# Kernel optimization log

Hardware: AMD Instinct MI355X
Metric: run time of the kernel (lower is better)

## Reference

```python
import jax, jax.numpy as jnp
import numpy as np
import math

B, T, D, H = 4, 2048, 1024, 16
HD = D // H  # head dim = 64

def setup_inputs() -> dict:
    key = jax.random.key(0)
    ks = jax.random.split(key, 4)
    scale = 1.0 / math.sqrt(D)
    return {
        "x": jax.random.normal(ks[0], (B, T, D), dtype=jnp.float32),
        "Wq": jax.random.normal(ks[1], (D, D), dtype=jnp.float32) * scale,
        "bq": jnp.zeros((D,), dtype=jnp.float32),
        "Wk": jax.random.normal(ks[2], (D, D), dtype=jnp.float32) * scale,
        "bk": jnp.zeros((D,), dtype=jnp.float32),
        "Wv": jax.random.normal(ks[3], (D, D), dtype=jnp.float32) * scale,
        "bv": jnp.zeros((D,), dtype=jnp.float32),
    }

def reference(x, Wq, bq, Wk, bk, Wv, bv):
    b, t, d = x.shape
    # QKV projections (nn.Dense): x @ W + b
    q = x @ Wq + bq
    k = x @ Wk + bk
    v = x @ Wv + bv
    # b n (h d) -> b h n d
    def split_heads(y):
        return y.reshape(b, t, H, HD).transpose(0, 2, 1, 3)
    q, k, v = split_heads(q), split_heads(k), split_heads(v)
    # scaled dot-product attention; scale by sqrt(features // heads)
    scores = jnp.einsum("bhqd,bhkd->bhqk", q, k) / math.sqrt(HD)
    attn = jax.nn.softmax(scores, axis=-1)
    # dropout rate 0.0 / eval mode => identity
    out = jnp.einsum("bhqk,bhkd->bhqd", attn, v)
    # b h n d -> b n (h d)
    return out.transpose(0, 2, 1, 3).reshape(b, t, d)
```

## Files before the change

kernel.cpp:

```cpp
#include <hip/hip_runtime.h>
#include <math.h>

typedef unsigned short u16;
typedef short short8 __attribute__((ext_vector_type(8)));
typedef u16 u16x4 __attribute__((ext_vector_type(4)));
typedef float f32x4 __attribute__((ext_vector_type(4)));
typedef __bf16 bf16x8 __attribute__((ext_vector_type(8)));

#define B_ 4
#define T_ 2048
#define D_ 1024
#define H_ 16
#define HD_ 64
#define BT_ 8192

__device__ __forceinline__ u16 f2bf(float f) {
  unsigned u = __builtin_bit_cast(unsigned, f);
  u = u + 0x7fffu + ((u >> 16) & 1u);
  return (u16)(u >> 16);
}
__device__ __forceinline__ f32x4 mfma16(short8 a, short8 b, f32x4 c) {
  return __builtin_amdgcn_mfma_f32_16x16x32_bf16(
      __builtin_bit_cast(bf16x8, a), __builtin_bit_cast(bf16x8, b), c, 0, 0, 0);
}
__device__ __forceinline__ void async16(u16* lds, const u16* g) {
  __builtin_amdgcn_global_load_lds(
      (const __attribute__((address_space(1))) unsigned int*)g,
      (__attribute__((address_space(3))) unsigned int*)lds, 16, 0, 0);
}

__global__ __launch_bounds__(256) void prep(
    const float* __restrict__ x, const float* __restrict__ Wq,
    const float* __restrict__ Wk, const float* __restrict__ Wv,
    u16* __restrict__ xbf, u16* __restrict__ wtq, u16* __restrict__ wtk,
    u16* __restrict__ wtv) {
  __shared__ float sh[32][33];
  if (blockIdx.y < 256) {
    int bid = blockIdx.y * 32 + blockIdx.x;
    int i = (bid * 256 + threadIdx.x) * 4;
    float4 v = *(const float4*)&x[i];
    u16x4 o = {f2bf(v.x), f2bf(v.y), f2bf(v.z), f2bf(v.w)};
    *(u16x4*)&xbf[i] = o;
    return;
  }
  const int yy = blockIdx.y - 256;
  const int wsel = yy >> 5;
  const float* in = (wsel == 0) ? Wq : (wsel == 1) ? Wk : Wv;
  u16* out = (wsel == 0) ? wtq : (wsel == 1) ? wtk : wtv;
  const int bx = blockIdx.x * 32, by = (yy & 31) * 32;
  const int col = threadIdx.x & 31, r8 = threadIdx.x >> 5;
#pragma unroll
  for (int i = 0; i < 4; i++) {
    int row = r8 + i * 8;
    sh[row][col] = in[(size_t)(by + row) * 1024 + bx + col];
  }
  __syncthreads();
#pragma unroll
  for (int i = 0; i < 4; i++) {
    int row = r8 + i * 8;
    out[(size_t)(bx + row) * 1024 + by + col] = f2bf(sh[col][row]);
  }
}

__global__ __launch_bounds__(256, 2) void gemm_qkv3(
    const u16* __restrict__ xbf, const u16* __restrict__ wtq,
    const u16* __restrict__ wtk, const u16* __restrict__ wtv,
    const float* __restrict__ bq, const float* __restrict__ bk,
    const float* __restrict__ bv, u16* __restrict__ qh, u16* __restrict__ kh,
    u16* __restrict__ vth, float qscale) {
  __shared__ __align__(16) u16 Rs[2][128 * 64];
  __shared__ __align__(16) u16 Cs[2][128 * 64];
  const int proj = blockIdx.y >> 3;
  const int fy = blockIdx.y & 7;
  const u16* Rm;
  const u16* Cm;
  const float* bias;
  u16* out;
  float scale;
  int r0, c0, vmode;
  if (proj == 0) {
    Rm = wtq; Cm = xbf; bias = bq; out = qh; scale = qscale; vmode = 0;
    r0 = fy * 128; c0 = blockIdx.x * 128;
  } else if (proj == 1) {
    Rm = wtk; Cm = xbf; bias = bk; out = kh; scale = 1.0f; vmode = 0;
    r0 = fy * 128; c0 = blockIdx.x * 128;
  } else {
    Rm = xbf; Cm = wtv; bias = bv; out = vth; scale = 1.0f; vmode = 1;
    r0 = blockIdx.x * 128; c0 = fy * 128;
  }
  const int tid = threadIdx.x;
  const int lane = tid & 63;
  const int w = tid >> 6;
  const int wr = w >> 1, wc = w & 1;
  const int c = lane & 15, q4 = lane >> 4;
  const int cx7 = c & 7;

  f32x4 acc[4][4];
#pragma unroll
  for (int i = 0; i < 4; i++)
#pragma unroll
    for (int j = 0; j < 4; j++) {
      f32x4 z = {0.f, 0.f, 0.f, 0.f};
      acc[i][j] = z;
    }

  const int sr = tid >> 3, pc = tid & 7;

#pragma unroll
  for (int i = 0; i < 4; i++) {
    int row = i * 32 + sr;
    int sc = (pc ^ (row & 7)) * 8;
    async16(&Rs[0][(i * 256 + tid) * 8], &Rm[(size_t)(r0 + row) * 1024 + sc]);
    async16(&Cs[0][(i * 256 + tid) * 8], &Cm[(size_t)(c0 + row) * 1024 + sc]);
  }

  for (int ks = 0; ks < 16; ks++) {
    const int cur = ks & 1;
    __syncthreads();
    if (ks + 1 < 16) {
      const int kk = (ks + 1) * 64;
#pragma unroll
      for (int i = 0; i < 4; i++) {
        int row = i * 32 + sr;
        int sc = (pc ^ (row & 7)) * 8;
        async16(&Rs[cur ^ 1][(i * 256 + tid) * 8],
                &Rm[(size_t)(r0 + row) * 1024 + kk + sc]);
        async16(&Cs[cur ^ 1][(i * 256 + tid) * 8],
                &Cm[(size_t)(c0 + row) * 1024 + kk + sc]);
      }
    }
#pragma unroll
    for (int h = 0; h < 2; h++) {
      short8 rF[4], cF[4];
      const int ko = ((h * 4 + q4) ^ cx7) * 8;
#pragma unroll
      for (int i = 0; i < 4; i++)
        rF[i] = *(const short8*)&Rs[cur][(wr * 64 + i * 16 + c) * 64 + ko];
#pragma unroll
      for (int j = 0; j < 4; j++)
        cF[j] = *(const short8*)&Cs[cur][(wc * 64 + j * 16 + c) * 64 + ko];
#pragma unroll
      for (int i = 0; i < 4; i++)
#pragma unroll
        for (int j = 0; j < 4; j++) acc[i][j] = mfma16(rF[i], cF[j], acc[i][j]);
    }
  }

  if (vmode == 0) {
#pragma unroll
    for (int i = 0; i < 4; i++) {
      int ng = r0 + wr * 64 + i * 16 + q4 * 4;
      int h = ng >> 6, hd = ng & 63;
#pragma unroll
      for (int j = 0; j < 4; j++) {
        int tg = c0 + wc * 64 + j * 16 + c;
        int b = tg >> 11, tt = tg & 2047;
        u16x4 o;
#pragma unroll
        for (int r = 0; r < 4; r++)
          o[r] = f2bf((acc[i][j][r] + bias[ng + r]) * scale);
        *(u16x4*)&out[(((size_t)(b * 16 + h) * 2048 + tt) << 6) + hd] = o;
      }
    }
  } else {
#pragma unroll
    for (int i = 0; i < 4; i++) {
      int tg = r0 + wr * 64 + i * 16 + q4 * 4;
      int b = tg >> 11, tt = tg & 2047;
      int tp = (tt & ~63) | (((tt >> 2) & 3) << 4) | (((tt >> 4) & 3) << 2);
#pragma unroll
      for (int j = 0; j < 4; j++) {
        int ng = c0 + wc * 64 + j * 16 + c;
        int h = ng >> 6, hd = ng & 63;
        float bb = bias[ng];
        u16x4 o;
#pragma unroll
        for (int r = 0; r < 4; r++) o[r] = f2bf(acc[i][j][r] + bb);
        *(u16x4*)&out[((size_t)((b * 16 + h) * 64 + hd)) * 2048 + tp] = o;
      }
    }
  }
}

__global__ __launch_bounds__(256, 2) void attn_fused(const u16* __restrict__ Qh,
                                                     const u16* __restrict__ Kh,
                                                     const u16* __restrict__ VTh,
                                                     float* __restrict__ out) {
  __shared__ __align__(16) u16 Ks[2][64 * 64];
  __shared__ __align__(16) u16 VTs[2][64 * 64];
  const int tid = threadIdx.x;
  const int w = tid >> 6, lane = tid & 63;
  const int c = lane & 15, q4 = lane >> 4;
  const int cx7 = c & 7;
  const int qt = blockIdx.x, bh = blockIdx.y;

  short8 qf[4][2];
#pragma unroll
  for (int nblk = 0; nblk < 4; nblk++) {
    const u16* Qp =
        Qh + ((size_t)bh * T_ + qt * 256 + w * 64 + nblk * 16 + c) * 64;
    qf[nblk][0] = *(const short8*)&Qp[q4 * 8];
    qf[nblk][1] = *(const short8*)&Qp[32 + q4 * 8];
  }

  const u16* Kb = Kh + (size_t)bh * T_ * 64;
  const u16* Vb = VTh + (size_t)bh * 64 * T_;

  f32x4 O[4][4];
#pragma unroll
  for (int nblk = 0; nblk < 4; nblk++)
#pragma unroll
    for (int nb = 0; nb < 4; nb++) {
      f32x4 z = {0.f, 0.f, 0.f, 0.f};
      O[nblk][nb] = z;
    }
  float lsum[4] = {0.f, 0.f, 0.f, 0.f};

  const int sr = tid >> 3, pc = tid & 7;

#pragma unroll
  for (int i = 0; i < 2; i++) {
    int r = i * 32 + sr;
    int sc = (pc ^ (r & 7)) * 8;
    async16(&Ks[0][(i * 256 + tid) * 8], &Kb[(size_t)r * 64 + sc]);
    async16(&VTs[0][(i * 256 + tid) * 8], &Vb[(size_t)r * T_ + sc]);
  }

  for (int it = 0; it < T_ / 64; it++) {
    const int cur = it & 1;
    __syncthreads();
    if (it + 1 < T_ / 64) {
      const int kt = (it + 1) * 64;
#pragma unroll
      for (int i = 0; i < 2; i++) {
        int r = i * 32 + sr;
        int sc = (pc ^ (r & 7)) * 8;
        async16(&Ks[cur ^ 1][(i * 256 + tid) * 8],
                &Kb[(size_t)(kt + r) * 64 + sc]);
        async16(&VTs[cur ^ 1][(i * 256 + tid) * 8],
                &Vb[(size_t)r * T_ + kt + sc]);
      }
    }

#pragma unroll
    for (int p = 0; p < 2; p++) {
      f32x4 S[2][4];
#pragma unroll
      for (int kbi = 0; kbi < 2; kbi++) {
        const int kb = p * 2 + kbi;
        short8 k0 =
            *(const short8*)&Ks[cur][(kb * 16 + c) * 64 + ((q4 ^ cx7) * 8)];
        short8 k1 = *(const short8*)&Ks[cur][(kb * 16 + c) * 64 +
                                             (((4 + q4) ^ cx7) * 8)];
#pragma unroll
        for (int nblk = 0; nblk < 4; nblk++) {
          f32x4 z = {0.f, 0.f, 0.f, 0.f};
          S[kbi][nblk] = mfma16(k0, qf[nblk][0], z);
          S[kbi][nblk] = mfma16(k1, qf[nblk][1], S[kbi][nblk]);
        }
      }

      short8 pf8[4];
#pragma unroll
      for (int nblk = 0; nblk < 4; nblk++) {
        float e[8];
#pragma unroll
        for (int kbi = 0; kbi < 2; kbi++)
#pragma unroll
          for (int r = 0; r < 4; r++)
            e[kbi * 4 + r] = __builtin_amdgcn_exp2f(S[kbi][nblk][r]);
        lsum[nblk] += ((e[0] + e[1]) + (e[2] + e[3])) +
                      ((e[4] + e[5]) + (e[6] + e[7]));
        bf16x8 t = {(__bf16)e[0], (__bf16)e[1], (__bf16)e[2], (__bf16)e[3],
                    (__bf16)e[4], (__bf16)e[5], (__bf16)e[6], (__bf16)e[7]};
        pf8[nblk] = __builtin_bit_cast(short8, t);
      }

#pragma unroll
      for (int nb = 0; nb < 4; nb++) {
        short8 vf = *(const short8*)&VTs[cur][(nb * 16 + c) * 64 +
                                              (((q4 * 2 + p) ^ cx7) * 8)];
#pragma unroll
        for (int nblk = 0; nblk < 4; nblk++)
          O[nblk][nb] = mfma16(pf8[nblk], vf, O[nblk][nb]);
      }
    }
  }

#pragma unroll
  for (int nblk = 0; nblk < 4; nblk++) {
    lsum[nblk] += __shfl_xor(lsum[nblk], 16);
    lsum[nblk] += __shfl_xor(lsum[nblk], 32);
  }

  const int bq = bh >> 4, h = bh & 15;
#pragma unroll
  for (int nblk = 0; nblk < 4; nblk++)
#pragma unroll
    for (int r = 0; r < 4; r++) {
      float rl = 1.0f / __shfl(lsum[nblk], q4 * 4 + r);
      int t = qt * 256 + w * 64 + nblk * 16 + q4 * 4 + r;
#pragma unroll
      for (int nb = 0; nb < 4; nb++)
        out[((size_t)(bq * T_ + t)) * 1024 + h * 64 + nb * 16 + c] =
            O[nblk][nb][r] * rl;
    }
}

extern "C" void kernel_launch(void* const* d_in, const int* in_sizes, int n_in,
                              void* d_out, int out_size, void* d_ws, size_t ws_size,
                              hipStream_t stream) {
  (void)in_sizes; (void)n_in; (void)out_size; (void)ws_size;
  const float* x  = (const float*)d_in[0];
  const float* Wq = (const float*)d_in[1];
  const float* bq = (const float*)d_in[2];
  const float* Wk = (const float*)d_in[3];
  const float* bk = (const float*)d_in[4];
  const float* Wv = (const float*)d_in[5];
  const float* bv = (const float*)d_in[6];
  float* out = (float*)d_out;

  u16* ob  = (u16*)d_out;
  u16* xbf = ob;
  u16* wtq = ob + (size_t)BT_ * D_;
  u16* wtk = wtq + (size_t)D_ * D_;
  u16* wtv = wtk + (size_t)D_ * D_;

  u16* ws  = (u16*)d_ws;
  u16* qh  = ws;
  u16* kh  = qh + (size_t)BT_ * D_;
  u16* vth = kh + (size_t)BT_ * D_;

  prep<<<dim3(32, 352), 256, 0, stream>>>(x, Wq, Wk, Wv, xbf, wtq, wtk, wtv);

  const float qscale = 0.125f * 1.44269504088896f;
  gemm_qkv3<<<dim3(64, 24), 256, 0, stream>>>(xbf, wtq, wtk, wtv, bq, bk, bv,
                                              qh, kh, vth, qscale);

  attn_fused<<<dim3(8, 64), 256, 0, stream>>>(qh, kh, vth, out);
}
```

Measured before the change: 228.8 us.

## Enlarge QKV GEMM tiles to 256x256 with 8-wave interleaved staging and setprio

The fused QKV projection GEMM moves from 128x128 tiles with 4 waves to 256x256 tiles with 8 waves, 128KB of dynamic shared memory and a double-buffered schedule. Global-to-LDS loads for the next K-step are interleaved between four MFMA sub-blocks, separated by explicit barriers, with s_setprio raised around MFMA bursts. The aim is more data reuse per load and better overlap of memory traffic with matrix math. The cost is one block per CU because of the LDS footprint, and a 384-block grid that leaves an uneven tail wave.

```diff
diff --git a/kernel.cpp b/kernel.cpp
--- a/kernel.cpp
+++ b/kernel.cpp
@@ -62,16 +62,18 @@
   }
 }
 
-__global__ __launch_bounds__(256, 2) void gemm_qkv3(
+__global__ __launch_bounds__(512, 2) void gemm_qkv3(
     const u16* __restrict__ xbf, const u16* __restrict__ wtq,
     const u16* __restrict__ wtk, const u16* __restrict__ wtv,
     const float* __restrict__ bq, const float* __restrict__ bk,
     const float* __restrict__ bv, u16* __restrict__ qh, u16* __restrict__ kh,
     u16* __restrict__ vth, float qscale) {
-  __shared__ __align__(16) u16 Rs[2][128 * 64];
-  __shared__ __align__(16) u16 Cs[2][128 * 64];
-  const int proj = blockIdx.y >> 3;
-  const int fy = blockIdx.y & 7;
+  extern __shared__ __align__(16) u16 smem[];
+  u16* As = smem;
+  u16* Bs = smem + 32768;
+
+  const int proj = blockIdx.y >> 2;
+  const int fy = blockIdx.y & 3;
   const u16* Rm;
   const u16* Cm;
   const float* bias;
@@ -80,102 +82,167 @@
   int r0, c0, vmode;
   if (proj == 0) {
     Rm = wtq; Cm = xbf; bias = bq; out = qh; scale = qscale; vmode = 0;
-    r0 = fy * 128; c0 = blockIdx.x * 128;
+    r0 = fy * 256; c0 = blockIdx.x * 256;
   } else if (proj == 1) {
     Rm = wtk; Cm = xbf; bias = bk; out = kh; scale = 1.0f; vmode = 0;
-    r0 = fy * 128; c0 = blockIdx.x * 128;
+    r0 = fy * 256; c0 = blockIdx.x * 256;
   } else {
     Rm = xbf; Cm = wtv; bias = bv; out = vth; scale = 1.0f; vmode = 1;
-    r0 = blockIdx.x * 128; c0 = fy * 128;
+    r0 = blockIdx.x * 256; c0 = fy * 256;
   }
   const int tid = threadIdx.x;
   const int lane = tid & 63;
   const int w = tid >> 6;
-  const int wr = w >> 1, wc = w & 1;
+  const int wr = w >> 2, wc = w & 3;
   const int c = lane & 15, q4 = lane >> 4;
   const int cx7 = c & 7;
-
-  f32x4 acc[4][4];
-#pragma unroll
-  for (int i = 0; i < 4; i++)
+  const int sr = tid >> 3, pc = tid & 7;
+  const int scx = (pc ^ (sr & 7)) * 8;
+  const int k0o = (q4 ^ cx7) * 8;
+  const int k1o = ((4 + q4) ^ cx7) * 8;
+  const int brow0 = (wc & 1) * 64;
+
+  f32x4 acc[8][4];
+#pragma unroll
+  for (int i = 0; i < 8; i++)
 #pragma unroll
     for (int j = 0; j < 4; j++) {
       f32x4 z = {0.f, 0.f, 0.f, 0.f};
       acc[i][j] = z;
     }
 
-  const int sr = tid >> 3, pc = tid & 7;
-
-#pragma unroll
-  for (int i = 0; i < 4; i++) {
-    int row = i * 32 + sr;
-    int sc = (pc ^ (row & 7)) * 8;
-    async16(&Rs[0][(i * 256 + tid) * 8], &Rm[(size_t)(r0 + row) * 1024 + sc]);
-    async16(&Cs[0][(i * 256 + tid) * 8], &Cm[(size_t)(c0 + row) * 1024 + sc]);
-  }
-
-  for (int ks = 0; ks < 16; ks++) {
-    const int cur = ks & 1;
-    __syncthreads();
-    if (ks + 1 < 16) {
-      const int kk = (ks + 1) * 64;
-#pragma unroll
-      for (int i = 0; i < 4; i++) {
-        int row = i * 32 + sr;
-        int sc = (pc ^ (row & 7)) * 8;
-        async16(&Rs[cur ^ 1][(i * 256 + tid) * 8],
-                &Rm[(size_t)(r0 + row) * 1024 + kk + sc]);
-        async16(&Cs[cur ^ 1][(i * 256 + tid) * 8],
-                &Cm[(size_t)(c0 + row) * 1024 + kk + sc]);
-      }
-    }
-#pragma unroll
-    for (int h = 0; h < 2; h++) {
-      short8 rF[4], cF[4];
-      const int ko = ((h * 4 + q4) ^ cx7) * 8;
-#pragma unroll
-      for (int i = 0; i < 4; i++)
-        rF[i] = *(const short8*)&Rs[cur][(wr * 64 + i * 16 + c) * 64 + ko];
-#pragma unroll
-      for (int j = 0; j < 4; j++)
-        cF[j] = *(const short8*)&Cs[cur][(wc * 64 + j * 16 + c) * 64 + ko];
-#pragma unroll
-      for (int i = 0; i < 4; i++)
-#pragma unroll
-        for (int j = 0; j < 4; j++) acc[i][j] = mfma16(rF[i], cF[j], acc[i][j]);
-    }
-  }
+#define STAGE_A(n, h)                                                        \
+  {                                                                          \
+    const u16* s_ = Rm + (size_t)(r0 + (h)*128 + sr) * 1024 + (n)*64 + scx;  \
+    u16* d_ = As + ((((n)&1) * 2 + (h)) * 8192) + tid * 8;                   \
+    async16(d_, s_);                                                         \
+    async16(d_ + 4096, s_ + (size_t)64 * 1024);                              \
+  }
+#define STAGE_B(n, h)                                                        \
+  {                                                                          \
+    const u16* s_ = Cm + (size_t)(c0 + (h)*128 + sr) * 1024 + (n)*64 + scx;  \
+    u16* d_ = Bs + ((((n)&1) * 2 + (h)) * 8192) + tid * 8;                   \
+    async16(d_, s_);                                                         \
+    async16(d_ + 4096, s_ + (size_t)64 * 1024);                              \
+  }
+
+  STAGE_B(0, 0); STAGE_A(0, 0); STAGE_B(0, 1); STAGE_A(0, 1);
+  STAGE_B(1, 0); STAGE_A(1, 0);
+  asm volatile("s_waitcnt vmcnt(4)" ::: "memory");
+  asm volatile("s_barrier" ::: "memory");
+
+#pragma unroll 2
+  for (int n = 0; n < 16; ++n) {
+    const u16* Aslot = As + (((n & 1) * 2 + wr) * 8192);
+    const u16* Bslot = Bs + (((n & 1) * 2 + (wc >> 1)) * 8192);
+    short8 aF[4][2], bF[4][2];
+
+#pragma unroll
+    for (int ii = 0; ii < 4; ii++) {
+      aF[ii][0] = *(const short8*)&Aslot[(ii * 16 + c) * 64 + k0o];
+      aF[ii][1] = *(const short8*)&Aslot[(ii * 16 + c) * 64 + k1o];
+    }
+#pragma unroll
+    for (int jj = 0; jj < 2; jj++) {
+      bF[jj][0] = *(const short8*)&Bslot[(brow0 + jj * 16 + c) * 64 + k0o];
+      bF[jj][1] = *(const short8*)&Bslot[(brow0 + jj * 16 + c) * 64 + k1o];
+    }
+    STAGE_B((n + 1) & 15, 1);
+    asm volatile("s_barrier" ::: "memory");
+    __builtin_amdgcn_s_setprio(1);
+#pragma unroll
+    for (int ii = 0; ii < 4; ii++)
+#pragma unroll
+      for (int jj = 0; jj < 2; jj++) {
+        acc[ii][jj] = mfma16(aF[ii][0], bF[jj][0], acc[ii][jj]);
+        acc[ii][jj] = mfma16(aF[ii][1], bF[jj][1], acc[ii][jj]);
+      }
+    __builtin_amdgcn_s_setprio(0);
+    asm volatile("s_barrier" ::: "memory");
+
+#pragma unroll
+    for (int jj = 2; jj < 4; jj++) {
+      bF[jj][0] = *(const short8*)&Bslot[(brow0 + jj * 16 + c) * 64 + k0o];
+      bF[jj][1] = *(const short8*)&Bslot[(brow0 + jj * 16 + c) * 64 + k1o];
+    }
+    STAGE_A((n + 1) & 15, 1);
+    asm volatile("s_barrier" ::: "memory");
+    __builtin_amdgcn_s_setprio(1);
+#pragma unroll
+    for (int ii = 0; ii < 4; ii++)
+#pragma unroll
+      for (int jj = 2; jj < 4; jj++) {
+        acc[ii][jj] = mfma16(aF[ii][0], bF[jj][0], acc[ii][jj]);
+        acc[ii][jj] = mfma16(aF[ii][1], bF[jj][1], acc[ii][jj]);
+      }
+    __builtin_amdgcn_s_setprio(0);
+    asm volatile("s_barrier" ::: "memory");
+
+#pragma unroll
+    for (int ii = 0; ii < 4; ii++) {
+      aF[ii][0] = *(const short8*)&Aslot[((4 + ii) * 16 + c) * 64 + k0o];
+      aF[ii][1] = *(const short8*)&Aslot[((4 + ii) * 16 + c) * 64 + k1o];
+    }
+    STAGE_B((n + 2) & 15, 0);
+    asm volatile("s_barrier" ::: "memory");
+    __builtin_amdgcn_s_setprio(1);
+#pragma unroll
+    for (int ii = 0; ii < 4; ii++)
+#pragma unroll
+      for (int jj = 0; jj < 2; jj++) {
+        acc[4 + ii][jj] = mfma16(aF[ii][0], bF[jj][0], acc[4 + ii][jj]);
+        acc[4 + ii][jj] = mfma16(aF[ii][1], bF[jj][1], acc[4 + ii][jj]);
+      }
+    __builtin_amdgcn_s_setprio(0);
+    asm volatile("s_barrier" ::: "memory");
+
+    STAGE_A((n + 2) & 15, 0);
+    asm volatile("s_barrier" ::: "memory");
+    __builtin_amdgcn_s_setprio(1);
+#pragma unroll
+    for (int ii = 0; ii < 4; ii++)
+#pragma unroll
+      for (int jj = 2; jj < 4; jj++) {
+        acc[4 + ii][jj] = mfma16(aF[ii][0], bF[jj][0], acc[4 + ii][jj]);
+        acc[4 + ii][jj] = mfma16(aF[ii][1], bF[jj][1], acc[4 + ii][jj]);
+      }
+    __builtin_amdgcn_s_setprio(0);
+    asm volatile("s_waitcnt vmcnt(4)" ::: "memory");
+    asm volatile("s_barrier" ::: "memory");
+  }
+#undef STAGE_A
+#undef STAGE_B
 
   if (vmode == 0) {
 #pragma unroll
-    for (int i = 0; i < 4; i++) {
-      int ng = r0 + wr * 64 + i * 16 + q4 * 4;
+    for (int mi = 0; mi < 8; mi++) {
+      int ng = r0 + wr * 128 + mi * 16 + q4 * 4;
       int h = ng >> 6, hd = ng & 63;
 #pragma unroll
-      for (int j = 0; j < 4; j++) {
-        int tg = c0 + wc * 64 + j * 16 + c;
+      for (int ni = 0; ni < 4; ni++) {
+        int tg = c0 + wc * 64 + ni * 16 + c;
         int b = tg >> 11, tt = tg & 2047;
         u16x4 o;
 #pragma unroll
         for (int r = 0; r < 4; r++)
-          o[r] = f2bf((acc[i][j][r] + bias[ng + r]) * scale);
+          o[r] = f2bf((acc[mi][ni][r] + bias[ng + r]) * scale);
         *(u16x4*)&out[(((size_t)(b * 16 + h) * 2048 + tt) << 6) + hd] = o;
       }
     }
   } else {
 #pragma unroll
-    for (int i = 0; i < 4; i++) {
-      int tg = r0 + wr * 64 + i * 16 + q4 * 4;
+    for (int mi = 0; mi < 8; mi++) {
+      int tg = r0 + wr * 128 + mi * 16 + q4 * 4;
       int b = tg >> 11, tt = tg & 2047;
       int tp = (tt & ~63) | (((tt >> 2) & 3) << 4) | (((tt >> 4) & 3) << 2);
 #pragma unroll
-      for (int j = 0; j < 4; j++) {
-        int ng = c0 + wc * 64 + j * 16 + c;
+      for (int ni = 0; ni < 4; ni++) {
+        int ng = c0 + wc * 64 + ni * 16 + c;
         int h = ng >> 6, hd = ng & 63;
         float bb = bias[ng];
         u16x4 o;
 #pragma unroll
-        for (int r = 0; r < 4; r++) o[r] = f2bf(acc[i][j][r] + bb);
+        for (int r = 0; r < 4; r++) o[r] = f2bf(acc[mi][ni][r] + bb);
         *(u16x4*)&out[((size_t)((b * 16 + h) * 64 + hd)) * 2048 + tp] = o;
       }
     }
@@ -334,8 +401,8 @@
   prep<<<dim3(32, 352), 256, 0, stream>>>(x, Wq, Wk, Wv, xbf, wtq, wtk, wtv);
 
   const float qscale = 0.125f * 1.44269504088896f;
-  gemm_qkv3<<<dim3(64, 24), 256, 0, stream>>>(xbf, wtq, wtk, wtv, bq, bk, bv,
-                                              qh, kh, vth, qscale);
+  gemm_qkv3<<<dim3(32, 12), 512, 131072, stream>>>(xbf, wtq, wtk, wtv, bq, bk,
+                                                   bv, qh, kh, vth, qscale);
 
   attn_fused<<<dim3(8, 64), 256, 0, stream>>>(qh, kh, vth, out);
 }
```

Measured after the change: 225.0 us, median of 3. No clear change (-1.6%).
